# Performance work log

Measured on AMD Instinct MI355X. Metric: run time of the kernel, lower is better.

Reference implementation:

```python
import jax, jax.numpy as jnp
import numpy as np

C = 128          # feature_num
INHI_RANGE = C // 8 + 1   # 17, banded channel window width
HALF = INHI_RANGE // 2    # 8


def conv2d(x, w, b=None, pad=0):
    # x: [N,C,H,W], w: [O,I,kh,kw]
    y = jax.lax.conv_general_dilated(
        x, w, window_strides=(1, 1), padding=[(pad, pad), (pad, pad)],
        dimension_numbers=("NCHW", "OIHW", "NCHW"))
    if b is not None:
        y = y + b[None, :, None, None]
    return y


def maxpool(x, k, s, pad):
    # torch MaxPool2d pads with -inf
    return jax.lax.reduce_window(
        x, -jnp.inf, jax.lax.max,
        window_dimensions=(1, 1, k, k), window_strides=(1, 1, s, s),
        padding=[(0, 0), (0, 0), (pad, pad), (pad, pad)])


def lrn(x):
    # Banded cross-channel inhibition: for channel i, sum x^2 over channels
    # j in [i-HALF, i+HALF] (clamped). Original code does this as a dense
    # (128,C,C) bmm; here it is a windowed channel reduction via cumsum.
    # NOTE: the torch code detaches y (x.clone().detach()), so the
    # denominator is a constant w.r.t. autodiff -> stop_gradient.
    x2 = jax.lax.stop_gradient(x) ** 2                      # [N,C,H,W]
    cs = jnp.cumsum(x2, axis=1)
    cs = jnp.concatenate([jnp.zeros_like(cs[:, :1]), cs], axis=1)  # [N,C+1,H,W]
    idx = jnp.arange(C)
    hi = jnp.minimum(idx + HALF + 1, C)
    lo = jnp.maximum(idx - HALF, 0)
    y = cs[:, hi] - cs[:, lo]                               # windowed sum
    y = (y * (0.001 / INHI_RANGE) + 1.0) ** 0.75
    return x / y


def rcl(x, fw, fb, rw, iters=3):
    f = conv2d(x, fw, fb, pad=1)
    r = lrn(jax.nn.relu(f))
    for _ in range(iters):
        r = lrn(jax.nn.relu(f + conv2d(r, rw, None, pad=1)))
    return r


def setup_inputs() -> dict:
    key = jax.random.key(0)
    ks = jax.random.split(key, 20)
    d = {}
    d["x"] = jax.random.normal(ks[0], (128, 3, 64, 64), jnp.float32)
    d["conv1_w"] = jax.random.normal(ks[1], (C, 3, 5, 5), jnp.float32) * 0.05
    d["conv1_b"] = jnp.zeros((C,), jnp.float32)
    d["bn_g"] = jnp.ones((C,), jnp.float32)
    d["bn_b"] = jnp.zeros((C,), jnp.float32)
    for i, n in enumerate(["2", "3", "4", "5"]):
        d[f"f{n}_w"] = jax.random.normal(ks[2 + 3 * i], (C, C, 3, 3), jnp.float32) * 0.02
        d[f"f{n}_b"] = jnp.zeros((C,), jnp.float32)
        d[f"r{n}_w"] = jax.random.normal(ks[3 + 3 * i], (C, C, 3, 3), jnp.float32) * 0.02
    d["mlp_w"] = jax.random.normal(ks[18], (10, C), jnp.float32) * 0.05
    d["mlp_b"] = jnp.zeros((10,), jnp.float32)
    return d


def reference(x, conv1_w, conv1_b, bn_g, bn_b,
              f2_w, f2_b, r2_w, f3_w, f3_b, r3_w,
              f4_w, f4_b, r4_w, f5_w, f5_b, r5_w,
              mlp_w, mlp_b):
    h = conv2d(x, conv1_w, conv1_b, pad=2)                  # [128,C,64,64]
    # BatchNorm2d (training-mode batch statistics, eps=1e-5)
    mean = h.mean(axis=(0, 2, 3), keepdims=True)
    var = h.var(axis=(0, 2, 3), keepdims=True)
    h = (h - mean) * jax.lax.rsqrt(var + 1e-5)
    h = h * bn_g[None, :, None, None] + bn_b[None, :, None, None]
    h = jax.nn.relu(h)
    h = maxpool(h, 3, 2, 1)                                 # 64 -> 32
    h = rcl(h, f2_w, f2_b, r2_w)                            # dropout = identity (eval)
    h = rcl(h, f3_w, f3_b, r3_w)
    h = maxpool(h, 3, 2, 1)                                 # 32 -> 16
    h = rcl(h, f4_w, f4_b, r4_w)
    h = rcl(h, f5_w, f5_b, r5_w)
    h = maxpool(h, 3, 2, 0)                                 # 16 -> 7
    y = h.max(axis=(2, 3))                                  # global max pool [128,C]
    return y @ mlp_w.T + mlp_b
```

## Files before the change

kernel.cpp:

```cpp
#include <hip/hip_runtime.h>


#define CCH 128
constexpr float KAPPA = 0.001f / 17.0f;

typedef __attribute__((ext_vector_type(8))) _Float16 half8;
typedef __attribute__((ext_vector_type(4))) float f32x4;

union U4 { uint4 v; ushort us[8]; _Float16 h[8]; half8 f; };
union U2 { ushort4 u; _Float16 h[4]; };

__global__ __launch_bounds__(256) void zero_stats(float* __restrict__ s) {
    s[threadIdx.x] = 0.f;
}

__global__ __launch_bounds__(256) void wcvt1(const float* __restrict__ wsrc,
                                             _Float16* __restrict__ wdst)
{
    const int idx = blockIdx.x * 256 + threadIdx.x;
    const int kc = idx >> 12;
    const int rem = idx & 4095;
    const int co = rem >> 5;
    const int kk = rem & 31;
    const int k = kc * 32 + kk;
    wdst[idx] = (k < 75) ? (_Float16)wsrc[co * 75 + k] : (_Float16)0.f;
}

__global__ __launch_bounds__(256, 2) void conv1m(
    const float* __restrict__ x, const _Float16* __restrict__ wc1,
    const float* __restrict__ bias, float* __restrict__ stats,
    _Float16* __restrict__ ph, _Float16* __restrict__ pp)
{
    __shared__ _Float16 xst[3 * 8 * 68];
    __shared__ _Float16 bnc[4 * 64 * 128];
    __shared__ float ps[4][128], ps2[4][128];

    const int bid = blockIdx.x;
    const int n = bid & 127;
    const int strip = bid >> 7;
    const int y0 = strip * 4;
    const int tid = threadIdx.x;
    const int w = tid >> 6, l = tid & 63;
    const int l15 = l & 15, lg = l >> 4;

    const float* xn = x + (size_t)n * 3 * 4096;
    for (int i = tid; i < 3 * 8 * 68; i += 256) {
        int ci = i / (8 * 68);
        int rm = i - ci * (8 * 68);
        int r = rm / 68, c = rm - r * 68;
        int gy = y0 - 2 + r, gx = c - 2;
        float v = ((unsigned)gy < 64u && (unsigned)gx < 64u)
                      ? xn[ci * 4096 + gy * 64 + gx] : 0.f;
        xst[i] = (_Float16)v;
    }

    f32x4 acc[8][4];
    #pragma unroll
    for (int cot = 0; cot < 8; ++cot) {
        f32x4 bv = *(const f32x4*)&bias[cot * 16 + lg * 4];
        #pragma unroll
        for (int pt = 0; pt < 4; ++pt) acc[cot][pt] = bv;
    }
    __syncthreads();

    #pragma unroll
    for (int kc = 0; kc < 3; ++kc) {
        int ba[8];
        #pragma unroll
        for (int j = 0; j < 8; ++j) {
            int k = kc * 32 + lg * 8 + j;
            k = k > 74 ? 74 : k;
            int ci = k / 25;
            int r = k - ci * 25;
            int ky = r / 5;
            int kx = r - ky * 5;
            ba[j] = (ci * 8 + w + ky) * 68 + l15 + kx;
        }
        half8 bf[4];
        #pragma unroll
        for (int pt = 0; pt < 4; ++pt) {
            U4 bb;
            #pragma unroll
            for (int j = 0; j < 8; ++j) bb.h[j] = xst[ba[j] + pt * 16];
            bf[pt] = bb.f;
        }
        const _Float16* wk = wc1 + kc * 4096 + l15 * 32 + lg * 8;
        #pragma unroll
        for (int cot = 0; cot < 8; ++cot) {
            half8 av = *(const half8*)&wk[cot * 512];
            #pragma unroll
            for (int pt = 0; pt < 4; ++pt)
                acc[cot][pt] = __builtin_amdgcn_mfma_f32_16x16x32_f16(
                    av, bf[pt], acc[cot][pt], 0, 0, 0);
        }
    }

    #pragma unroll
    for (int cot = 0; cot < 8; ++cot) {
        float s[4] = {0.f, 0.f, 0.f, 0.f}, s2[4] = {0.f, 0.f, 0.f, 0.f};
        #pragma unroll
        for (int pt = 0; pt < 4; ++pt)
            #pragma unroll
            for (int j = 0; j < 4; ++j) {
                float v = acc[cot][pt][j];
                s[j] += v; s2[j] += v * v;
            }
        #pragma unroll
        for (int o = 1; o < 16; o <<= 1)
            #pragma unroll
            for (int j = 0; j < 4; ++j) {
                s[j]  += __shfl_xor(s[j], o, 64);
                s2[j] += __shfl_xor(s2[j], o, 64);
            }
        if (l15 == 0) {
            #pragma unroll
            for (int j = 0; j < 4; ++j) {
                ps[w][cot * 16 + lg * 4 + j] = s[j];
                ps2[w][cot * 16 + lg * 4 + j] = s2[j];
            }
        }
    }

    #pragma unroll
    for (int cot = 0; cot < 8; ++cot)
        #pragma unroll
        for (int pt = 0; pt < 4; ++pt) {
            int c = pt * 16 + l15;
            int colx = (cot * 16 + lg * 4) ^ ((c & 7) * 8);
            U2 pk;
            pk.h[0] = (_Float16)acc[cot][pt][0];
            pk.h[1] = (_Float16)acc[cot][pt][1];
            pk.h[2] = (_Float16)acc[cot][pt][2];
            pk.h[3] = (_Float16)acc[cot][pt][3];
            *(ushort4*)&bnc[(w * 64 + c) * 128 + colx] = pk.u;
        }
    __syncthreads();

    if (tid < 128) {
        float A = ps[0][tid] + ps[1][tid] + ps[2][tid] + ps[3][tid];
        float B = ps2[0][tid] + ps2[1][tid] + ps2[2][tid] + ps2[3][tid];
        atomicAdd(&stats[tid], A);
        atomicAdd(&stats[tid + 128], B);
    }

    constexpr float NEG = -3.0e38f;
    #pragma unroll
    for (int i = 0; i < 6; ++i) {
        int t = tid + i * 256;
        if (t < 1024) {
            int cg = t & 15, ox = (t >> 4) & 31, oysel = t >> 9;
            float m[8];
            #pragma unroll
            for (int j = 0; j < 8; ++j) m[j] = NEG;
            #pragma unroll
            for (int dy = 0; dy < 3; ++dy) {
                int r = 2 * oysel - 1 + dy;
                if (r < 0) continue;
                #pragma unroll
                for (int dx = 0; dx < 3; ++dx) {
                    int c = 2 * ox - 1 + dx;
                    if ((unsigned)c >= 64u) continue;
                    U4 v;
                    v.v = *(const uint4*)&bnc[(r * 64 + c) * 128 + ((cg * 8) ^ ((c & 7) * 8))];
                    #pragma unroll
                    for (int j = 0; j < 8; ++j) m[j] = fmaxf(m[j], (float)v.h[j]);
                }
            }
            U4 o;
            #pragma unroll
            for (int j = 0; j < 8; ++j) o.h[j] = (_Float16)m[j];
            int oy = strip * 2 + oysel;
            *(uint4*)&ph[((size_t)n * 1024 + oy * 32 + ox) * 128 + cg * 8] = o.v;
        } else if (strip < 15) {
            int t2 = t - 1024;
            int cg = t2 & 15, ox = (t2 >> 4) & 31;
            float m[8];
            #pragma unroll
            for (int j = 0; j < 8; ++j) m[j] = NEG;
            #pragma unroll
            for (int dx = 0; dx < 3; ++dx) {
                int c = 2 * ox - 1 + dx;
                if ((unsigned)c >= 64u) continue;
                U4 v;
                v.v = *(const uint4*)&bnc[(3 * 64 + c) * 128 + ((cg * 8) ^ ((c & 7) * 8))];
                #pragma unroll
                for (int j = 0; j < 8; ++j) m[j] = fmaxf(m[j], (float)v.h[j]);
            }
            U4 o;
            #pragma unroll
            for (int j = 0; j < 8; ++j) o.h[j] = (_Float16)m[j];
            *(uint4*)&pp[(((size_t)n * 15 + strip) * 32 + ox) * 128 + cg * 8] = o.v;
        }
    }
}

__global__ __launch_bounds__(256) void pool_fixr(const _Float16* __restrict__ pp,
                                                 _Float16* __restrict__ ph)
{
    const int idx = blockIdx.x * 256 + threadIdx.x;
    const int cg = idx & 15;
    const int ox = (idx >> 4) & 31;
    const int t = idx >> 9;
    const int s = t % 15;
    const int n = t / 15;
    const _Float16* p = pp + (((size_t)n * 15 + s) * 32 + ox) * 128 + cg * 8;
    _Float16* a = ph + ((size_t)n * 1024 + (2 * s + 2) * 32 + ox) * 128 + cg * 8;
    U4 av, bv;
    av.v = *(const uint4*)a;
    bv.v = *(const uint4*)p;
    #pragma unroll
    for (int j = 0; j < 8; ++j)
        if ((float)bv.h[j] > (float)av.h[j]) av.h[j] = bv.h[j];
    *(uint4*)a = av.v;
}

__global__ __launch_bounds__(128) void bn_finalize(
    const float* __restrict__ stats, const float* __restrict__ g,
    const float* __restrict__ b, float* __restrict__ scsh)
{
    const int c = threadIdx.x;
    const float M = 128.f * 4096.f;
    float mean = stats[c] / M;
    float var = stats[c + 128] / M - mean * mean;
    float rstd = rsqrtf(var + 1e-5f);
    float sc = g[c] * rstd;
    scsh[c] = sc;
    scsh[c + 128] = b[c] - mean * sc;
}

__global__ __launch_bounds__(256) void bnrelu(
    const _Float16* __restrict__ ph, const float* __restrict__ scsh,
    _Float16* __restrict__ out)
{
    const int idx = blockIdx.x * 256 + threadIdx.x;
    const int cg = idx & 15;
    const size_t e = (size_t)(idx >> 4) * 128 + cg * 8;
    U4 v; v.v = *(const uint4*)&ph[e];
    U4 o;
    #pragma unroll
    for (int j = 0; j < 8; ++j) {
        int co = cg * 8 + j;
        float f = (float)v.h[j] * scsh[co] + scsh[co + 128];
        o.h[j] = (_Float16)fmaxf(f, 0.f);
    }
    *(uint4*)&out[e] = o.v;
}

__global__ __launch_bounds__(256) void wcvt(const float* __restrict__ wsrc,
                                            _Float16* __restrict__ wdst)
{
    const int idx = blockIdx.x * 256 + threadIdx.x;
    const int t = idx >> 14;
    const int rem = idx & 16383;
    const int co = rem >> 7;
    const int ci = rem & 127;
    wdst[idx] = (_Float16)wsrc[(co * 128 + ci) * 9 + t];
}

template<int H, bool ADD_F>
__global__ __launch_bounds__(512, 4) void conv3f(
    const _Float16* __restrict__ in, const _Float16* __restrict__ wb,
    const float* __restrict__ bias, _Float16* __restrict__ fbuf,
    _Float16* __restrict__ outp)
{
    constexpr int W = H, HW = H * W;
    constexpr int XP = W + 2;
    constexpr int PITCH = 40;
    constexpr int ROWS = 10;
    constexpr int PTN = W / 8;
    constexpr int BLKPX = 8 * W;
    constexpr int STAGE = ROWS * XP * PITCH;
    constexpr int TASKS = ROWS * W * 4;
    constexpr int NIT = (TASKS + 511) / 512;
    constexpr int LOG4W = (H == 32) ? 7 : 6;
    constexpr int LDSH = BLKPX * 128;
    constexpr int CPL = LDSH / (512 * 8);
    constexpr int LOGPX = (H == 32) ? 8 : 7;
    constexpr int NSUB = 512 / BLKPX;
    constexpr int SEGO = 128 / NSUB;
    constexpr int LEN = SEGO + 16;
    constexpr int NSV = LEN / 8;

    __shared__ _Float16 xs[LDSH];

    const int bid = blockIdx.x;
    const int slot = bid >> 3;
    const int n = (bid & 7) + 8 * (slot & 15);
    const int y0 = (slot >> 4) * 8;
    const int tid = threadIdx.x;
    const int w = tid >> 6, l = tid & 63;
    const int rp = w & 3, wh = w >> 2;
    const int l15 = l & 15, lg = l >> 4;

    for (int i = tid; i < STAGE / 2; i += 512) ((uint*)xs)[i] = 0;

    f32x4 acc[4][PTN];
    #pragma unroll
    for (int a = 0; a < 4; ++a) {
        f32x4 bv = {0.f, 0.f, 0.f, 0.f};
        if constexpr (!ADD_F) bv = *(const f32x4*)&bias[(wh * 4 + a) * 16 + lg * 4];
        #pragma unroll
        for (int pt = 0; pt < PTN; ++pt) acc[a][pt] = bv;
    }

    const _Float16* inb = in + (size_t)n * HW * 128;
    const size_t gblk = ((size_t)n * HW + (size_t)y0 * W) * 128;
    uint4 stg[NIT];

    auto issue = [&](int c0) {
        #pragma unroll
        for (int i = 0; i < NIT; ++i) {
            int t = tid + i * 512;
            uint4 v = {0u, 0u, 0u, 0u};
            if (TASKS % 512 == 0 || t < TASKS) {
                int g = t & 3, xx = (t >> 2) & (W - 1), yl = t >> LOG4W;
                int gy = y0 - 1 + yl;
                if ((unsigned)gy < (unsigned)H)
                    v = *(const uint4*)&inb[((size_t)(gy * W + xx)) * 128 + c0 + g * 8];
            }
            stg[i] = v;
        }
    };
    auto commit = [&]() {
        #pragma unroll
        for (int i = 0; i < NIT; ++i) {
            int t = tid + i * 512;
            if (TASKS % 512 == 0 || t < TASKS) {
                int g = t & 3, xx = (t >> 2) & (W - 1), yl = t >> LOG4W;
                *(uint4*)&xs[(yl * XP + xx + 1) * PITCH + g * 8] = stg[i];
            }
        }
    };

    int bofs[PTN];
    #pragma unroll
    for (int pt = 0; pt < PTN; ++pt) {
        int row_l = 2 * rp + ((H == 32) ? (pt >> 1) : pt);
        int xb = ((H == 32) ? (pt & 1) * 16 : 0) + l15;
        bofs[pt] = ((row_l + 1) * XP + xb + 1) * PITCH + lg * 8;
    }
    const _Float16* wl = wb + l15 * 128 + lg * 8;

    issue(0);
    for (int cc = 0; cc < 4; ++cc) {
        const int c0 = cc * 32;
        __syncthreads();
        commit();
        if (cc < 3) issue(c0 + 32);
        __syncthreads();
        #pragma unroll
        for (int ky = -1; ky <= 1; ++ky)
            #pragma unroll
            for (int kx = -1; kx <= 1; ++kx) {
                const int t9 = (ky + 1) * 3 + (kx + 1);
                half8 bf[PTN];
                #pragma unroll
                for (int pt = 0; pt < PTN; ++pt)
                    bf[pt] = *(const half8*)&xs[bofs[pt] + (ky * XP + kx) * PITCH];
                const _Float16* wt = wl + t9 * 16384 + c0;
                half8 av[4];
                #pragma unroll
                for (int a = 0; a < 4; ++a)
                    av[a] = *(const half8*)&wt[(wh * 4 + a) * 2048];
                #pragma unroll
                for (int a = 0; a < 4; ++a)
                    #pragma unroll
                    for (int pt = 0; pt < PTN; ++pt)
                        acc[a][pt] = __builtin_amdgcn_mfma_f32_16x16x32_f16(
                            av[a], bf[pt], acc[a][pt], 0, 0, 0);
            }
    }

    __syncthreads();

    if constexpr (ADD_F) {
        #pragma unroll
        for (int i = 0; i < CPL; ++i) {
            int gidx = i * 512 + tid;
            int px = gidx >> 4, cu = gidx & 15;
            uint4 v = *(const uint4*)&fbuf[gblk + (size_t)gidx * 8];
            *(uint4*)&xs[px * 128 + ((cu ^ (px & 7)) * 8)] = v;
        }
        __syncthreads();
    }

    #pragma unroll
    for (int a = 0; a < 4; ++a)
        #pragma unroll
        for (int pt = 0; pt < PTN; ++pt) {
            const int bpx = (H == 32)
                ? (2 * rp + (pt >> 1)) * 32 + (pt & 1) * 16 + l15
                : (2 * rp + pt) * 16 + l15;
            const int ch = wh * 64 + a * 16 + lg * 4;
            const int col = ch ^ ((bpx & 7) * 8);
            U2 pk;
            if constexpr (ADD_F) {
                U2 cur; cur.u = *(const ushort4*)&xs[bpx * 128 + col];
                pk.h[0] = (_Float16)(acc[a][pt][0] + (float)cur.h[0]);
                pk.h[1] = (_Float16)(acc[a][pt][1] + (float)cur.h[1]);
                pk.h[2] = (_Float16)(acc[a][pt][2] + (float)cur.h[2]);
                pk.h[3] = (_Float16)(acc[a][pt][3] + (float)cur.h[3]);
            } else {
                pk.h[0] = (_Float16)acc[a][pt][0];
                pk.h[1] = (_Float16)acc[a][pt][1];
                pk.h[2] = (_Float16)acc[a][pt][2];
                pk.h[3] = (_Float16)acc[a][pt][3];
            }
            *(ushort4*)&xs[bpx * 128 + col] = pk.u;
        }
    __syncthreads();

    if constexpr (!ADD_F) {
        #pragma unroll
        for (int i = 0; i < CPL; ++i) {
            int gidx = i * 512 + tid;
            int px = gidx >> 4, cu = gidx & 15;
            uint4 v = *(const uint4*)&xs[px * 128 + ((cu ^ (px & 7)) * 8)];
            *(uint4*)&fbuf[gblk + (size_t)gidx * 8] = v;
        }
    }

    const int px = tid & (BLKPX - 1);
    const int seg = tid >> LOGPX;
    const int p3 = px & 7;
    const int cstart = seg ? (SEGO * seg - 8) : 0;
    const int gb0 = cstart >> 3;
    const int zlim = 128 - cstart;
    const int wlo = seg ? 16 : 8;
    const int whi = wlo + SEGO;

    U4 sv[NSV];
    #pragma unroll
    for (int i = 0; i < NSV; ++i) {
        int g = gb0 + i; g = g > 15 ? 15 : g;
        sv[i].v = *(const uint4*)&xs[px * 128 + ((g ^ p3) * 8)];
    }
    __syncthreads();

    {
        float ring[17], zr[9], wsum = 0.f;
        #pragma unroll
        for (int i = 0; i < 17; ++i) ring[i] = 0.f;
        #pragma unroll
        for (int i = 0; i < 9; ++i) zr[i] = 0.f;
        U4 ob;
        #pragma unroll
        for (int cl = 0; cl < LEN; ++cl) {
            float v = (float)sv[cl >> 3].h[cl & 7];
            float z = (cl < zlim && v > 0.f) ? v : 0.f;
            float zz = z * z;
            wsum += zz - ring[cl % 17];
            ring[cl % 17] = zz;
            zr[cl % 9] = z;
            if (cl >= 8) {
                const int q = (cl - 8) & 7;
                float p75 = exp2f(-0.75f * log2f(wsum * KAPPA + 1.f));
                ob.h[q] = (_Float16)(zr[(cl + 1) % 9] * p75);
                if (q == 7 && cl >= wlo && cl < whi) {
                    const int o7 = cstart + cl - 15;
                    *(uint4*)&xs[px * 128 + (((o7 >> 3) ^ p3) * 8)] = ob.v;
                }
            }
        }
    }
    __syncthreads();

    #pragma unroll
    for (int i = 0; i < CPL; ++i) {
        int gidx = i * 512 + tid;
        int px2 = gidx >> 4, cu = gidx & 15;
        uint4 v = *(const uint4*)&xs[px2 * 128 + ((cu ^ (px2 & 7)) * 8)];
        *(uint4*)&outp[gblk + (size_t)gidx * 8] = v;
    }
}

__global__ __launch_bounds__(256) void pool32v(const _Float16* __restrict__ in,
                                               _Float16* __restrict__ out)
{
    const int idx = blockIdx.x * 256 + threadIdx.x;
    const int cg = idx & 15;
    const int opix = (idx >> 4) & 255;
    const int n = idx >> 12;
    const int oy = opix >> 4, ox = opix & 15;
    const _Float16* ib = in + (size_t)n * 1024 * 128 + cg * 8;
    float m[8] = {0.f, 0.f, 0.f, 0.f, 0.f, 0.f, 0.f, 0.f};
    #pragma unroll
    for (int dy = -1; dy <= 1; ++dy) {
        int iy = 2 * oy + dy;
        if ((unsigned)iy >= 32u) continue;
        #pragma unroll
        for (int dx = -1; dx <= 1; ++dx) {
            int ix = 2 * ox + dx;
            if ((unsigned)ix >= 32u) continue;
            U4 v; v.v = *(const uint4*)&ib[(size_t)(iy * 32 + ix) * 128];
            #pragma unroll
            for (int i = 0; i < 8; ++i) m[i] = fmaxf(m[i], (float)v.h[i]);
        }
    }
    U4 o;
    #pragma unroll
    for (int i = 0; i < 8; ++i) o.h[i] = (_Float16)m[i];
    *(uint4*)&out[((size_t)n * 256 + opix) * 128 + cg * 8] = o.v;
}

__global__ __launch_bounds__(256) void gmax2(const _Float16* __restrict__ in,
                                             float* __restrict__ g)
{
    const int idx = blockIdx.x * 256 + threadIdx.x;
    const int c8 = idx & 15;
    const int n = idx >> 4;
    const _Float16* ib = in + (size_t)n * 256 * 128 + c8 * 8;
    float m[8] = {0.f, 0.f, 0.f, 0.f, 0.f, 0.f, 0.f, 0.f};
    for (int y = 0; y < 15; ++y)
        #pragma unroll
        for (int x = 0; x < 15; ++x) {
            U4 v; v.v = *(const uint4*)&ib[(size_t)(y * 16 + x) * 128];
            #pragma unroll
            for (int i = 0; i < 8; ++i) m[i] = fmaxf(m[i], (float)v.h[i]);
        }
    float* gb = g + n * 128 + c8 * 8;
    *(float4*)&gb[0] = {m[0], m[1], m[2], m[3]};
    *(float4*)&gb[4] = {m[4], m[5], m[6], m[7]};
}

__global__ __launch_bounds__(256) void mlp_k(
    const float* __restrict__ g, const float* __restrict__ w,
    const float* __restrict__ b, float* __restrict__ out)
{
    const int idx = blockIdx.x * 256 + threadIdx.x;
    if (idx >= 1280) return;
    const int n = idx / 10, k = idx - n * 10;
    float acc = b[k];
    for (int c = 0; c < CCH; ++c) acc += g[n * CCH + c] * w[k * CCH + c];
    out[idx] = acc;
}

extern "C" void kernel_launch(void* const* d_in, const int* in_sizes, int n_in,
                              void* d_out, int out_size, void* d_ws, size_t ws_size,
                              hipStream_t stream)
{
    const float* x   = (const float*)d_in[0];
    const float* w1  = (const float*)d_in[1];
    const float* b1  = (const float*)d_in[2];
    const float* bng = (const float*)d_in[3];
    const float* bnb = (const float*)d_in[4];
    const float* fw[4] = {(const float*)d_in[5],  (const float*)d_in[8],
                          (const float*)d_in[11], (const float*)d_in[14]};
    const float* fb[4] = {(const float*)d_in[6],  (const float*)d_in[9],
                          (const float*)d_in[12], (const float*)d_in[15]};
    const float* rw[4] = {(const float*)d_in[7],  (const float*)d_in[10],
                          (const float*)d_in[13], (const float*)d_in[16]};
    const float* mw = (const float*)d_in[17];
    const float* mb = (const float*)d_in[18];
    float* out = (float*)d_out;

    _Float16* ws16 = (_Float16*)d_ws;
    _Float16* buf0 = ws16;
    _Float16* buf1 = ws16 + 16777216;
    _Float16* Fb32 = ws16 + 2 * 16777216;
    _Float16* base3 = ws16 + 3 * 16777216;
    _Float16* A16a = base3;
    _Float16* A16b = base3 + 4194304;
    _Float16* F16  = base3 + 2 * 4194304;
    _Float16* Wb   = base3 + 3 * 4194304;
    float* stats = (float*)(Wb + 8 * 147456);
    float* scsh  = stats + 256;
    float* gm    = scsh + 256;
    _Float16* Pp  = (_Float16*)(gm + 16384);
    _Float16* Wc1 = Pp + 7864320;
    _Float16* PH  = buf1;

    zero_stats<<<1, 256, 0, stream>>>(stats);
    wcvt1<<<48, 256, 0, stream>>>(w1, Wc1);
    conv1m<<<2048, 256, 0, stream>>>(x, Wc1, b1, stats, PH, Pp);
    pool_fixr<<<3840, 256, 0, stream>>>(Pp, PH);
    bn_finalize<<<1, 128, 0, stream>>>(stats, bng, bnb, scsh);
    bnrelu<<<8192, 256, 0, stream>>>(PH, scsh, buf0);

    const float* lw[8] = {fw[0], rw[0], fw[1], rw[1], fw[2], rw[2], fw[3], rw[3]};
    for (int i = 0; i < 8; ++i)
        wcvt<<<576, 256, 0, stream>>>(lw[i], Wb + i * 147456);

    _Float16* cur = buf0;
    _Float16* alt = buf1;
    for (int s = 0; s < 2; ++s) {
        conv3f<32, false><<<512, 512, 0, stream>>>(cur, Wb + (2*s) * 147456, fb[s], Fb32, alt);
        { _Float16* t = cur; cur = alt; alt = t; }
        for (int it = 0; it < 3; ++it) {
            conv3f<32, true><<<512, 512, 0, stream>>>(cur, Wb + (2*s+1) * 147456, nullptr, Fb32, alt);
            { _Float16* t = cur; cur = alt; alt = t; }
        }
    }
    pool32v<<<2048, 256, 0, stream>>>(cur, A16a);

    _Float16* cur16 = A16a;
    _Float16* alt16 = A16b;
    for (int s = 2; s < 4; ++s) {
        conv3f<16, false><<<256, 512, 0, stream>>>(cur16, Wb + (2*s) * 147456, fb[s], F16, alt16);
        { _Float16* t = cur16; cur16 = alt16; alt16 = t; }
        for (int it = 0; it < 3; ++it) {
            conv3f<16, true><<<256, 512, 0, stream>>>(cur16, Wb + (2*s+1) * 147456, nullptr, F16, alt16);
            { _Float16* t = cur16; cur16 = alt16; alt16 = t; }
        }
    }
    gmax2<<<8, 256, 0, stream>>>(cur16, gm);
    mlp_k<<<5, 256, 0, stream>>>(gm, mw, mb, out);
}
```

Baseline: 1.385 ms.

## Double-buffer conv3f input staging, use nontemporal memory ops, store LRN output directly

The conv3f kernel now stages input channel chunks into two LDS buffers, so the next chunk is committed while the current one is consumed. This cuts the syncs per chunk from two to one. Global loads and stores of activations and fbuf use nontemporal hints to avoid polluting cache. The LRN result is written straight from registers to global memory, dropping the LDS bounce, two barriers and the final copy loop. The cost is a larger LDS allocation, which may reduce occupancy at H=16, and per-thread 16-byte stores that may coalesce less well.

```diff
diff --git a/kernel.cpp b/kernel.cpp
--- a/kernel.cpp
+++ b/kernel.cpp
@@ -6,9 +6,19 @@
 
 typedef __attribute__((ext_vector_type(8))) _Float16 half8;
 typedef __attribute__((ext_vector_type(4))) float f32x4;
+typedef __attribute__((ext_vector_type(4))) uint u32x4;
 
 union U4 { uint4 v; ushort us[8]; _Float16 h[8]; half8 f; };
 union U2 { ushort4 u; _Float16 h[4]; };
+
+__device__ __forceinline__ uint4 nt_load4(const void* p) {
+    u32x4 t = __builtin_nontemporal_load((const u32x4*)p);
+    uint4 r; r.x = t.x; r.y = t.y; r.z = t.z; r.w = t.w; return r;
+}
+__device__ __forceinline__ void nt_store4(const uint4 v, void* p) {
+    u32x4 t = {v.x, v.y, v.z, v.w};
+    __builtin_nontemporal_store(t, (u32x4*)p);
+}
 
 __global__ __launch_bounds__(256) void zero_stats(float* __restrict__ s) {
     s[threadIdx.x] = 0.f;
@@ -273,8 +283,9 @@
     constexpr int TASKS = ROWS * W * 4;
     constexpr int NIT = (TASKS + 511) / 512;
     constexpr int LOG4W = (H == 32) ? 7 : 6;
-    constexpr int LDSH = BLKPX * 128;
-    constexpr int CPL = LDSH / (512 * 8);
+    constexpr int BOUNCE = BLKPX * 128;
+    constexpr int LDSH = (2 * STAGE > BOUNCE) ? 2 * STAGE : BOUNCE;
+    constexpr int CPL = BOUNCE / (512 * 8);
     constexpr int LOGPX = (H == 32) ? 8 : 7;
     constexpr int NSUB = 512 / BLKPX;
     constexpr int SEGO = 128 / NSUB;
@@ -292,7 +303,7 @@
     const int rp = w & 3, wh = w >> 2;
     const int l15 = l & 15, lg = l >> 4;
 
-    for (int i = tid; i < STAGE / 2; i += 512) ((uint*)xs)[i] = 0;
+    for (int i = tid; i < STAGE; i += 512) ((uint*)xs)[i] = 0;
 
     f32x4 acc[4][PTN];
     #pragma unroll
@@ -316,18 +327,18 @@
                 int g = t & 3, xx = (t >> 2) & (W - 1), yl = t >> LOG4W;
                 int gy = y0 - 1 + yl;
                 if ((unsigned)gy < (unsigned)H)
-                    v = *(const uint4*)&inb[((size_t)(gy * W + xx)) * 128 + c0 + g * 8];
+                    v = nt_load4(&inb[((size_t)(gy * W + xx)) * 128 + c0 + g * 8]);
             }
             stg[i] = v;
         }
     };
-    auto commit = [&]() {
+    auto commit = [&](int b) {
         #pragma unroll
         for (int i = 0; i < NIT; ++i) {
             int t = tid + i * 512;
             if (TASKS % 512 == 0 || t < TASKS) {
                 int g = t & 3, xx = (t >> 2) & (W - 1), yl = t >> LOG4W;
-                *(uint4*)&xs[(yl * XP + xx + 1) * PITCH + g * 8] = stg[i];
+                *(uint4*)&xs[b * STAGE + (yl * XP + xx + 1) * PITCH + g * 8] = stg[i];
             }
         }
     };
@@ -342,12 +353,13 @@
     const _Float16* wl = wb + l15 * 128 + lg * 8;
 
     issue(0);
+    commit(0);
+    issue(32);
+    __syncthreads();
+
     for (int cc = 0; cc < 4; ++cc) {
+        const int bo = (cc & 1) * STAGE;
         const int c0 = cc * 32;
-        __syncthreads();
-        commit();
-        if (cc < 3) issue(c0 + 32);
-        __syncthreads();
         #pragma unroll
         for (int ky = -1; ky <= 1; ++ky)
             #pragma unroll
@@ -356,7 +368,7 @@
                 half8 bf[PTN];
                 #pragma unroll
                 for (int pt = 0; pt < PTN; ++pt)
-                    bf[pt] = *(const half8*)&xs[bofs[pt] + (ky * XP + kx) * PITCH];
+                    bf[pt] = *(const half8*)&xs[bo + bofs[pt] + (ky * XP + kx) * PITCH];
                 const _Float16* wt = wl + t9 * 16384 + c0;
                 half8 av[4];
                 #pragma unroll
@@ -369,16 +381,17 @@
                         acc[a][pt] = __builtin_amdgcn_mfma_f32_16x16x32_f16(
                             av[a], bf[pt], acc[a][pt], 0, 0, 0);
             }
-    }
-
-    __syncthreads();
+        if (cc < 3) commit((cc + 1) & 1);
+        if (cc < 2) issue((cc + 2) * 32);
+        __syncthreads();
+    }
 
     if constexpr (ADD_F) {
         #pragma unroll
         for (int i = 0; i < CPL; ++i) {
             int gidx = i * 512 + tid;
             int px = gidx >> 4, cu = gidx & 15;
-            uint4 v = *(const uint4*)&fbuf[gblk + (size_t)gidx * 8];
+            uint4 v = nt_load4(&fbuf[gblk + (size_t)gidx * 8]);
             *(uint4*)&xs[px * 128 + ((cu ^ (px & 7)) * 8)] = v;
         }
         __syncthreads();
@@ -416,7 +429,7 @@
             int gidx = i * 512 + tid;
             int px = gidx >> 4, cu = gidx & 15;
             uint4 v = *(const uint4*)&xs[px * 128 + ((cu ^ (px & 7)) * 8)];
-            *(uint4*)&fbuf[gblk + (size_t)gidx * 8] = v;
+            nt_store4(v, &fbuf[gblk + (size_t)gidx * 8]);
         }
     }
 
@@ -428,6 +441,7 @@
     const int zlim = 128 - cstart;
     const int wlo = seg ? 16 : 8;
     const int whi = wlo + SEGO;
+    _Float16* opx = outp + gblk + (size_t)px * 128;
 
     U4 sv[NSV];
     #pragma unroll
@@ -435,7 +449,6 @@
         int g = gb0 + i; g = g > 15 ? 15 : g;
         sv[i].v = *(const uint4*)&xs[px * 128 + ((g ^ p3) * 8)];
     }
-    __syncthreads();
 
     {
         float ring[17], zr[9], wsum = 0.f;
@@ -458,19 +471,10 @@
                 ob.h[q] = (_Float16)(zr[(cl + 1) % 9] * p75);
                 if (q == 7 && cl >= wlo && cl < whi) {
                     const int o7 = cstart + cl - 15;
-                    *(uint4*)&xs[px * 128 + (((o7 >> 3) ^ p3) * 8)] = ob.v;
+                    nt_store4(ob.v, &opx[o7]);
                 }
             }
         }
-    }
-    __syncthreads();
-
-    #pragma unroll
-    for (int i = 0; i < CPL; ++i) {
-        int gidx = i * 512 + tid;
-        int px2 = gidx >> 4, cu = gidx & 15;
-        uint4 v = *(const uint4*)&xs[px2 * 128 + ((cu ^ (px2 & 7)) * 8)];
-        *(uint4*)&outp[gblk + (size_t)gidx * 8] = v;
     }
 }
 
```

After: 1.984 ms. +43.3%, slower.
